# Optimization experiments

Hardware: AMD Instinct MI355X
Metric: run time of the kernel (lower is better)

Reference implementation:

```python
import jax, jax.numpy as jnp
import numpy as np

DELTA_VAR = 0.5
DELTA_DIST = 1.5
VAR_WEIGHT = 1.0
DIST_WEIGHT = 1.0
REG_WEIGHT = 0.001
K = 16  # number of clusters (labels are in [0, K))


def setup_inputs() -> dict:
    key = jax.random.key(0)
    k1, k2 = jax.random.split(key)
    data = jax.random.normal(k1, (32, 512, 1024), dtype=jnp.float32)
    labels = jax.random.randint(k2, (512, 1024), 0, K, dtype=jnp.int32)
    return {"data": data, "labels": labels}


def reference(data, labels):
    D = data.shape[0]
    pts = data.reshape(D, -1).T          # [N, D] per-pixel embeddings
    lab = labels.reshape(-1)             # [N]

    # Per-cluster size and mean (center). All K clusters are present.
    counts = jax.ops.segment_sum(jnp.ones_like(lab, dtype=pts.dtype), lab,
                                 num_segments=K)          # [K]
    sums = jax.ops.segment_sum(pts, lab, num_segments=K)  # [K, D]
    centers = sums / counts[:, None]                      # [K, D]

    # Variance term: sum over all points of hinge(||center - x|| - dv)^2 / K
    diff = centers[lab] - pts                             # [N, D]
    dist = jnp.sqrt(jnp.sum(diff * diff, axis=-1))        # [N]
    var_term = jnp.sum(jnp.maximum(dist - DELTA_VAR, 0.0) ** 2) / K

    # Distance term: ordered pairs i != j of hinge(2*dd - ||ci - cj||)^2
    cd = centers[:, None, :] - centers[None, :, :]        # [K, K, D]
    sq = jnp.sum(cd * cd, axis=-1)                        # [K, K]
    eye = jnp.eye(K, dtype=bool)
    pd = jnp.sqrt(jnp.where(eye, 1.0, sq))                # safe sqrt on diag
    hinge = jnp.where(eye, 0.0, jnp.maximum(2.0 * DELTA_DIST - pd, 0.0) ** 2)
    dist_term = jnp.sum(hinge) / (K * (K - 1))

    # Regularization term: mean center norm
    reg_term = jnp.sum(jnp.sqrt(jnp.sum(centers * centers, axis=-1))) / K

    return VAR_WEIGHT * var_term + DIST_WEIGHT * dist_term + REG_WEIGHT * reg_term
```

## Files before the change

kernel.cpp:

```cpp
#include <hip/hip_runtime.h>


constexpr int KC = 16;
constexpr int DD = 32;
constexpr int NN = 512 * 1024;
constexpr int N4 = NN / 4;
constexpr int CHUNKS = 16;
constexpr int GROUPS_PER_CHUNK = N4 / CHUNKS;
constexpr int K1_ITERS = GROUPS_PER_CHUNK / 256;

__global__ __launch_bounds__(256) void k1_sums(const float4* __restrict__ data4,
                                               const int4* __restrict__ lab4,
                                               float* __restrict__ ws) {
    const int tid = threadIdx.x;
    const int d = blockIdx.y;
    const bool doCnt = (d == 0);

    __shared__ float acc[256 * 17];
    __shared__ float cnt[256 * 17];
    float* arow = acc + tid * 17;
    float* crow = cnt + tid * 17;
#pragma unroll
    for (int k = 0; k < KC; ++k) { arow[k] = 0.f; crow[k] = 0.f; }

    const int base = blockIdx.x * GROUPS_PER_CHUNK + tid;
    const float4* dplane = data4 + (size_t)d * N4;

    for (int it = 0; it < K1_ITERS; ++it) {
        const int g = base + it * 256;
        const float4 v = dplane[g];
        const int4 lb = lab4[g];
        arow[lb.x] += v.x;
        arow[lb.y] += v.y;
        arow[lb.z] += v.z;
        arow[lb.w] += v.w;
        if (doCnt) {
            crow[lb.x] += 1.f;
            crow[lb.y] += 1.f;
            crow[lb.z] += 1.f;
            crow[lb.w] += 1.f;
        }
    }
    __syncthreads();

    for (int off = 128; off > 0; off >>= 1) {
        if (tid < off) {
#pragma unroll
            for (int k = 0; k < KC; ++k) acc[tid * 17 + k] += acc[(tid + off) * 17 + k];
            if (doCnt) {
#pragma unroll
                for (int k = 0; k < KC; ++k) cnt[tid * 17 + k] += cnt[(tid + off) * 17 + k];
            }
        }
        __syncthreads();
    }
    if (tid < KC) {
        atomicAdd(&ws[tid * DD + d], acc[tid]);
        if (doCnt) atomicAdd(&ws[512 + tid], cnt[tid]);
    }
}

__global__ __launch_bounds__(256) void k2_centers(float* __restrict__ ws,
                                                  float* __restrict__ out) {
    __shared__ float cent[KC][DD + 1];
    __shared__ float red[256];
    const int tid = threadIdx.x;

    for (int idx = tid; idx < KC * DD; idx += 256) {
        const int k = idx >> 5, d = idx & 31;
        const float c = ws[idx] / ws[512 + k];
        cent[k][d] = c;
        ws[528 + d * KC + k] = c;
    }
    __syncthreads();

    const int i = tid >> 4, j = tid & 15;
    float sq = 0.f;
#pragma unroll
    for (int d = 0; d < DD; ++d) {
        const float df = cent[i][d] - cent[j][d];
        sq += df * df;
    }
    float val = 0.f;
    if (i != j) {
        const float pd = sqrtf(sq);
        const float t = fmaxf(3.0f - pd, 0.f);
        val = t * t * (1.0f / (KC * (KC - 1)));
    } else {
        float s2 = 0.f;
#pragma unroll
        for (int d = 0; d < DD; ++d) s2 += cent[i][d] * cent[i][d];
        val = sqrtf(s2) * (0.001f / KC);
    }
    red[tid] = val;
    __syncthreads();
    for (int off = 128; off > 0; off >>= 1) {
        if (tid < off) red[tid] += red[tid + off];
        __syncthreads();
    }
    if (tid == 0) out[0] = red[0];
}

__global__ __launch_bounds__(256) void k3_var(const float4* __restrict__ data4,
                                              const int4* __restrict__ lab4,
                                              const float* __restrict__ ws,
                                              float* __restrict__ out) {
    __shared__ float ct[DD * KC];
    const int tid = threadIdx.x;
    for (int idx = tid; idx < DD * KC; idx += 256) ct[idx] = ws[528 + idx];
    __syncthreads();

    const int g = blockIdx.x * 256 + tid;
    const int4 lb = lab4[g];
    float s0 = 0.f, s1 = 0.f, s2 = 0.f, s3 = 0.f;
#pragma unroll 8
    for (int d = 0; d < DD; ++d) {
        const float4 v = data4[(size_t)d * N4 + g];
        const float* ctd = ct + d * KC;
        const float d0 = ctd[lb.x] - v.x; s0 += d0 * d0;
        const float d1 = ctd[lb.y] - v.y; s1 += d1 * d1;
        const float d2 = ctd[lb.z] - v.z; s2 += d2 * d2;
        const float d3 = ctd[lb.w] - v.w; s3 += d3 * d3;
    }
    const float h0 = fmaxf(sqrtf(s0) - 0.5f, 0.f);
    const float h1 = fmaxf(sqrtf(s1) - 0.5f, 0.f);
    const float h2 = fmaxf(sqrtf(s2) - 0.5f, 0.f);
    const float h3 = fmaxf(sqrtf(s3) - 0.5f, 0.f);
    float lsum = h0 * h0 + h1 * h1 + h2 * h2 + h3 * h3;

#pragma unroll
    for (int off = 32; off > 0; off >>= 1) lsum += __shfl_down(lsum, off);
    __shared__ float wred[4];
    if ((tid & 63) == 0) wred[tid >> 6] = lsum;
    __syncthreads();
    if (tid == 0) {
        const float s = wred[0] + wred[1] + wred[2] + wred[3];
        atomicAdd(out, s * (1.0f / KC));
    }
}

extern "C" void kernel_launch(void* const* d_in, const int* in_sizes, int n_in,
                              void* d_out, int out_size, void* d_ws, size_t ws_size,
                              hipStream_t stream) {
    const float4* data4 = (const float4*)d_in[0];
    const int4* lab4 = (const int4*)d_in[1];
    float* out = (float*)d_out;
    float* ws = (float*)d_ws;

    hipMemsetAsync(ws, 0, 528 * sizeof(float), stream);

    k1_sums<<<dim3(CHUNKS, DD), 256, 0, stream>>>(data4, (const int4*)lab4, ws);
    k2_centers<<<1, 256, 0, stream>>>(ws, out);
    k3_var<<<512, 256, 0, stream>>>(data4, (const int4*)lab4, ws, out);
}
```

Baseline: 130.2 us.

## Use LDS atomics, parallel segment reduction, padded global atomics, duplicated center table

```diff
diff --git a/kernel.cpp b/kernel.cpp
--- a/kernel.cpp
+++ b/kernel.cpp
@@ -8,6 +8,11 @@
 constexpr int CHUNKS = 16;
 constexpr int GROUPS_PER_CHUNK = N4 / CHUNKS;
 constexpr int K1_ITERS = GROUPS_PER_CHUNK / 256;
+
+constexpr int WS_SUMS = 0;
+constexpr int WS_CNTS = 8192;
+constexpr int WS_CT2  = 8448;
+constexpr int WS_ZERO_FLOATS = 8448;
 
 __global__ __launch_bounds__(256) void k1_sums(const float4* __restrict__ data4,
                                                const int4* __restrict__ lab4,
@@ -21,7 +26,11 @@
     float* arow = acc + tid * 17;
     float* crow = cnt + tid * 17;
 #pragma unroll
-    for (int k = 0; k < KC; ++k) { arow[k] = 0.f; crow[k] = 0.f; }
+    for (int k = 0; k < KC; ++k) arow[k] = 0.f;
+    if (doCnt) {
+#pragma unroll
+        for (int k = 0; k < KC; ++k) crow[k] = 0.f;
+    }
 
     const int base = blockIdx.x * GROUPS_PER_CHUNK + tid;
     const float4* dplane = data4 + (size_t)d * N4;
@@ -30,33 +39,33 @@
         const int g = base + it * 256;
         const float4 v = dplane[g];
         const int4 lb = lab4[g];
-        arow[lb.x] += v.x;
-        arow[lb.y] += v.y;
-        arow[lb.z] += v.z;
-        arow[lb.w] += v.w;
+        atomicAdd(&arow[lb.x], v.x);
+        atomicAdd(&arow[lb.y], v.y);
+        atomicAdd(&arow[lb.z], v.z);
+        atomicAdd(&arow[lb.w], v.w);
         if (doCnt) {
-            crow[lb.x] += 1.f;
-            crow[lb.y] += 1.f;
-            crow[lb.z] += 1.f;
-            crow[lb.w] += 1.f;
+            atomicAdd(&crow[lb.x], 1.f);
+            atomicAdd(&crow[lb.y], 1.f);
+            atomicAdd(&crow[lb.z], 1.f);
+            atomicAdd(&crow[lb.w], 1.f);
         }
     }
     __syncthreads();
 
-    for (int off = 128; off > 0; off >>= 1) {
-        if (tid < off) {
+    const int k = tid >> 4, seg = tid & 15;
+    float s = 0.f;
 #pragma unroll
-            for (int k = 0; k < KC; ++k) acc[tid * 17 + k] += acc[(tid + off) * 17 + k];
-            if (doCnt) {
+    for (int i = 0; i < 16; ++i) s += acc[(seg * 16 + i) * 17 + k];
 #pragma unroll
-                for (int k = 0; k < KC; ++k) cnt[tid * 17 + k] += cnt[(tid + off) * 17 + k];
-            }
-        }
-        __syncthreads();
-    }
-    if (tid < KC) {
-        atomicAdd(&ws[tid * DD + d], acc[tid]);
-        if (doCnt) atomicAdd(&ws[512 + tid], cnt[tid]);
+    for (int off = 8; off > 0; off >>= 1) s += __shfl_down(s, off, 16);
+    if (seg == 0) atomicAdd(&ws[WS_SUMS + (k * DD + d) * 16], s);
+    if (doCnt) {
+        float c = 0.f;
+#pragma unroll
+        for (int i = 0; i < 16; ++i) c += cnt[(seg * 16 + i) * 17 + k];
+#pragma unroll
+        for (int off = 8; off > 0; off >>= 1) c += __shfl_down(c, off, 16);
+        if (seg == 0) atomicAdd(&ws[WS_CNTS + k * 16], c);
     }
 }
 
@@ -67,10 +76,11 @@
     const int tid = threadIdx.x;
 
     for (int idx = tid; idx < KC * DD; idx += 256) {
-        const int k = idx >> 5, d = idx & 31;
-        const float c = ws[idx] / ws[512 + k];
+        const int k = idx / DD, d = idx % DD;
+        const float c = ws[WS_SUMS + idx * 16] / ws[WS_CNTS + k * 16];
         cent[k][d] = c;
-        ws[528 + d * KC + k] = c;
+        ws[WS_CT2 + d * 32 + k] = c;
+        ws[WS_CT2 + d * 32 + 16 + k] = c;
     }
     __syncthreads();
 
@@ -105,22 +115,25 @@
                                               const int4* __restrict__ lab4,
                                               const float* __restrict__ ws,
                                               float* __restrict__ out) {
-    __shared__ float ct[DD * KC];
+    __shared__ float ct2[DD * 32];
     const int tid = threadIdx.x;
-    for (int idx = tid; idx < DD * KC; idx += 256) ct[idx] = ws[528 + idx];
+    for (int idx = tid; idx < DD * 32; idx += 256) ct2[idx] = ws[WS_CT2 + idx];
     __syncthreads();
 
     const int g = blockIdx.x * 256 + tid;
     const int4 lb = lab4[g];
+    const int dup = (tid & 32) >> 1;
+    const int o0 = lb.x + dup, o1 = lb.y + dup, o2 = lb.z + dup, o3 = lb.w + dup;
+
     float s0 = 0.f, s1 = 0.f, s2 = 0.f, s3 = 0.f;
 #pragma unroll 8
     for (int d = 0; d < DD; ++d) {
         const float4 v = data4[(size_t)d * N4 + g];
-        const float* ctd = ct + d * KC;
-        const float d0 = ctd[lb.x] - v.x; s0 += d0 * d0;
-        const float d1 = ctd[lb.y] - v.y; s1 += d1 * d1;
-        const float d2 = ctd[lb.z] - v.z; s2 += d2 * d2;
-        const float d3 = ctd[lb.w] - v.w; s3 += d3 * d3;
+        const float* ctd = ct2 + d * 32;
+        const float d0 = ctd[o0] - v.x; s0 += d0 * d0;
+        const float d1 = ctd[o1] - v.y; s1 += d1 * d1;
+        const float d2 = ctd[o2] - v.z; s2 += d2 * d2;
+        const float d3 = ctd[o3] - v.w; s3 += d3 * d3;
     }
     const float h0 = fmaxf(sqrtf(s0) - 0.5f, 0.f);
     const float h1 = fmaxf(sqrtf(s1) - 0.5f, 0.f);
@@ -147,9 +160,9 @@
     float* out = (float*)d_out;
     float* ws = (float*)d_ws;
 
-    hipMemsetAsync(ws, 0, 528 * sizeof(float), stream);
+    hipMemsetAsync(ws, 0, WS_ZERO_FLOATS * sizeof(float), stream);
 
-    k1_sums<<<dim3(CHUNKS, DD), 256, 0, stream>>>(data4, (const int4*)lab4, ws);
+    k1_sums<<<dim3(CHUNKS, DD), 256, 0, stream>>>(data4, lab4, ws);
     k2_centers<<<1, 256, 0, stream>>>(ws, out);
-    k3_var<<<512, 256, 0, stream>>>(data4, (const int4*)lab4, ws, out);
+    k3_var<<<512, 256, 0, stream>>>(data4, lab4, ws, out);
 }
```

New measurement: 226.9 us. 74.3% more time.
